# Optimization experiments

Hardware: AMD Instinct MI355X
Metric: run time of the kernel (lower is better)

Reference implementation:

```python
import jax, jax.numpy as jnp
import numpy as np

K = 20          # neighbors
EPS = 1e-5      # BatchNorm eps
SLOPE = 0.2     # LeakyReLU negative slope


def setup_inputs() -> dict:
    key = jax.random.key(0)
    k1, k2 = jax.random.split(key)
    B, C, N, O = 8, 64, 4096, 64
    x = jax.random.normal(k1, (B, C, N), dtype=jnp.float32)
    # 1x1 Conv2d(2C -> O, bias=False) kernel, squeezed to (O, 2C)
    W = jax.random.normal(k2, (O, 2 * C), dtype=jnp.float32) * 0.05
    gamma = jnp.ones((O,), jnp.float32)   # BN weight
    beta = jnp.zeros((O,), jnp.float32)   # BN bias
    return {"x": x, "W": W, "gamma": gamma, "beta": beta}


def _edgeconv(x, W, gamma, beta):
    B, C, N = x.shape
    xt = jnp.transpose(x, (0, 2, 1))                       # (B, N, C)
    # KNN on negative squared distance (matches torch topk of -dist)
    xx = jnp.sum(x * x, axis=1)                            # (B, N)
    inner = jnp.einsum('bnc,bmc->bnm', xt, xt)             # (B, N, N)
    neg_dist = 2.0 * inner - xx[:, :, None] - xx[:, None, :]
    _, idx = jax.lax.top_k(neg_dist, K)                    # (B, N, K) int32
    # gather neighbor features: nbr[b,n,k,c] = xt[b, idx[b,n,k], c]
    nbr = xt[jnp.arange(B)[:, None, None], idx]            # (B, N, K, C)
    center = jnp.broadcast_to(xt[:, :, None, :], (B, N, K, C))
    edge = jnp.concatenate([nbr - center, center], axis=-1)  # (B, N, K, 2C)
    # 1x1 conv == channel matmul
    y = jnp.einsum('bnkc,oc->bnko', edge, W)               # (B, N, K, O)
    # BatchNorm2d (training mode: batch statistics over B,N,K per channel)
    mean = jnp.mean(y, axis=(0, 1, 2))
    var = jnp.var(y, axis=(0, 1, 2))
    yn = (y - mean) * jax.lax.rsqrt(var + EPS) * gamma + beta
    ya = jnp.where(yn >= 0, yn, SLOPE * yn)                # LeakyReLU(0.2)
    out = jnp.max(ya, axis=2)                              # max over k -> (B, N, O)
    return jnp.transpose(out, (0, 2, 1))                   # (B, O, N)


def reference(x, W, gamma, beta):
    return _edgeconv(x, W, gamma, beta)
```

## Files before the change

### kernel.cpp

```cpp
#include <hip/hip_runtime.h>
#include <hip/hip_bf16.h>
#include <math.h>

#define B 8
#define C 64
#define NN 4096
#define O 64
#define KNN 20

typedef float f32x4 __attribute__((ext_vector_type(4)));
typedef short short8_t __attribute__((ext_vector_type(8)));

__device__ inline uint32_t fkey(float f) {
    uint32_t u = __float_as_uint(f);
    return u ^ (((uint32_t)((int32_t)u >> 31)) | 0x80000000u);
}

__device__ inline uint32_t med3u(uint32_t a, uint32_t b, uint32_t c) {
    uint32_t r;
    asm("v_med3_u32 %0, %1, %2, %3" : "=v"(r) : "v"(a), "v"(b), "v"(c));
    return r;
}
__device__ inline uint32_t umax(uint32_t a, uint32_t b) { return a > b ? a : b; }
__device__ inline uint32_t umin(uint32_t a, uint32_t b) { return a < b ? a : b; }

__device__ inline uint32_t minall16(uint32_t v) {
    uint32_t t;
    t = (uint32_t)__builtin_amdgcn_update_dpp(0, (int)v, 0x140, 0xF, 0xF, true);
    v = umin(v, t);
    t = (uint32_t)__builtin_amdgcn_update_dpp(0, (int)v, 0x141, 0xF, 0xF, true);
    v = umin(v, t);
    t = (uint32_t)__builtin_amdgcn_update_dpp(0, (int)v, 0x4E, 0xF, 0xF, true);
    v = umin(v, t);
    t = (uint32_t)__builtin_amdgcn_update_dpp(0, (int)v, 0xB1, 0xF, 0xF, true);
    v = umin(v, t);
    return v;
}


__global__ __launch_bounds__(256) void k1_split(const float* __restrict__ x,
                                                float* __restrict__ xt,
                                                __hip_bfloat16* __restrict__ xh,
                                                float* __restrict__ xx) {
    __shared__ float tile[64][65];
    int b  = blockIdx.x / (NN / 64);
    int n0 = (blockIdx.x % (NN / 64)) * 64;
    int t = threadIdx.x;
    #pragma unroll
    for (int it = 0; it < 16; ++it) {
        int i = it * 256 + t;
        int c = i >> 6, n = i & 63;
        tile[c][n] = x[(size_t)b * C * NN + (size_t)c * NN + n0 + n];
    }
    __syncthreads();
    #pragma unroll
    for (int it = 0; it < 16; ++it) {
        int i = it * 256 + t;
        int n = i >> 6, c = i & 63;
        float v = tile[c][n];
        xt[((size_t)(b * NN + n0 + n)) * C + c] = v;
        int tl   = (n0 + n) >> 4;
        int r    = n & 15;
        int half = c >> 5, cc = c & 31;
        int grp  = cc >> 3, e = cc & 7;
        size_t ta = (size_t)b * NN * 64 + (size_t)tl * 1024 + half * 512
                  + grp * 128 + r * 8 + e;
        xh[ta] = __float2bfloat16(v);
    }
    if (t < 64) {
        float s = 0.f;
        #pragma unroll
        for (int c = 0; c < 64; ++c) { float v = tile[c][t]; s = fmaf(v, v, s); }
        xx[(size_t)b * NN + t + n0] = s;
    }
}

__global__ __launch_bounds__(256) void k2_knn(const __hip_bfloat16* __restrict__ xh,
                                              const float* __restrict__ xt,
                                              const float* __restrict__ xx,
                                              int* __restrict__ idx) {
    int b     = blockIdx.x & 7;
    int qbase = (blockIdx.x >> 3) << 6;
    int t = threadIdx.x;
    int w = t >> 6, lane = t & 63;
    int laneid = lane & 15, grp = lane >> 4;
    int n0w = qbase + w * 16;

    const __hip_bfloat16* xhtb = xh + (size_t)b * NN * 64;
    const float* xxb = xx + (size_t)b * NN;
    const float* xtb = xt + (size_t)b * NN * 64;

    const __hip_bfloat16* lp = xhtb + lane * 8;

    {
    }
    short8_t Ah0 = *(const short8_t*)(lp + (size_t)(n0w >> 4) * 1024);
    short8_t Ah1 = *(const short8_t*)(lp + (size_t)(n0w >> 4) * 1024 + 512);

    float bq[4];
    #pragma unroll
    for (int j = 0; j < 4; ++j) bq[j] = -2.f - xxb[n0w + grp * 4 + j];

    uint32_t qq[4][12];
    #pragma unroll
    for (int j = 0; j < 4; ++j)
        #pragma unroll
        for (int i = 0; i < 12; ++i) qq[j][i] = 0xFFFFFFFFu;

    short8_t P00, P01, P10, P11, P20, P21, P30, P31;
    float Px0, Px1, Px2, Px3;
    P00 = *(const short8_t*)(lp);        P01 = *(const short8_t*)(lp + 512);
    P10 = *(const short8_t*)(lp + 1024); P11 = *(const short8_t*)(lp + 1536);
    P20 = *(const short8_t*)(lp + 2048); P21 = *(const short8_t*)(lp + 2560);
    P30 = *(const short8_t*)(lp + 3072); P31 = *(const short8_t*)(lp + 3584);
    Px0 = xxb[laneid];      Px1 = xxb[laneid + 16];
    Px2 = xxb[laneid + 32]; Px3 = xxb[laneid + 48];

#define SWEEP_BODY(PB0, PB1, PXX, K, PF, OFF)                                  \
    {                                                                          \
        float xxc = PXX;                                                       \
        f32x4 acc = {0.f, 0.f, 0.f, 0.f};                                      \
        acc = __builtin_amdgcn_mfma_f32_16x16x32_bf16(Ah0, PB0, acc, 0, 0, 0); \
        acc = __builtin_amdgcn_mfma_f32_16x16x32_bf16(Ah1, PB1, acc, 0, 0, 0); \
        PB0 = *(const short8_t*)(PF + OFF);                                    \
        PB1 = *(const short8_t*)(PF + OFF + 512);                              \
        PXX = xxb[ci0 + (4 + K) * 16];                                         \
        uint32_t ci = (uint32_t)(ci0 + K * 16);                                \
        _Pragma("unroll")                                                      \
        for (int j = 0; j < 4; ++j) {                                          \
            uint32_t u = __float_as_uint(fmaf(acc[j], 2.f, bq[j] - xxc));      \
            uint32_t nv = (u & 0xFFFFF000u) | ci;                              \
            _Pragma("unroll")                                                  \
            for (int i = 11; i >= 1; --i)                                      \
                qq[j][i] = med3u(qq[j][i - 1], qq[j][i], nv);                  \
            qq[j][0] = umin(qq[j][0], nv);                                     \
        }                                                                      \
    }

    #pragma unroll 1
    for (int tt = 0; tt < 256; tt += 4) {
        int ci0 = tt * 16 + laneid;
        const __hip_bfloat16* pf0 = lp + (size_t)(tt + 4) * 1024;
        const __hip_bfloat16* pf2 = pf0 + 2048;
        SWEEP_BODY(P00, P01, Px0, 0, pf0, 0)
        SWEEP_BODY(P10, P11, Px1, 1, pf0, 1024)
        SWEEP_BODY(P20, P21, Px2, 2, pf2, 0)
        SWEEP_BODY(P30, P31, Px3, 3, pf2, 1024)
    }
#undef SWEEP_BODY

    __shared__ uint32_t cand[4][16][33];
    __shared__ uint32_t rkk[4][16][33];
    __shared__ float qrow[4][16][68];

    #pragma unroll
    for (int i = 0; i < 16; ++i)
        qrow[w][i][lane] = xtb[(size_t)(n0w + i) * 64 + lane];

    #pragma unroll 1
    for (int r = 0; r < 32; ++r) {
        #pragma unroll
        for (int j = 0; j < 4; ++j) {
            uint32_t bk = minall16(qq[j][0]);
            bool win = (qq[j][0] == bk);
            #pragma unroll
            for (int i = 0; i < 11; ++i) qq[j][i] = win ? qq[j][i + 1] : qq[j][i];
            qq[j][11] = win ? 0xFFFFFFFFu : qq[j][11];
            if (laneid == 0) cand[w][grp * 4 + j][r] = bk & 4095u;
        }
    }
    __syncthreads();

    int rq = lane >> 2, rs = lane & 3;
    float qxx = xxb[n0w + rq];
    const float4* qr = (const float4*)qrow[w][rq];
    uint32_t ky[8], cl[8];
    #pragma unroll
    for (int e = 0; e < 8; ++e) {
        uint32_t col = cand[w][rq][rs + 4 * e];
        const float4* cr = (const float4*)(xtb + (size_t)col * 64);
        float a = 0.f;
        #pragma unroll
        for (int i = 0; i < 16; ++i) {
            float4 qv = qr[i], cv = cr[i];
            a = fmaf(qv.x, cv.x, a); a = fmaf(qv.y, cv.y, a);
            a = fmaf(qv.z, cv.z, a); a = fmaf(qv.w, cv.w, a);
        }
        float d = 2.f * a - qxx - xxb[col];
        ky[e] = fkey(d);
        cl[e] = col;
        rkk[w][rq][rs + 4 * e] = ky[e];
    }
    __syncthreads();

    int rank[8];
    #pragma unroll
    for (int e = 0; e < 8; ++e) rank[e] = 0;
    #pragma unroll
    for (int jj = 0; jj < 32; ++jj) {
        uint32_t kj = rkk[w][rq][jj], cj = cand[w][rq][jj];
        #pragma unroll
        for (int e = 0; e < 8; ++e)
            rank[e] += (kj > ky[e] || (kj == ky[e] && cj < cl[e])) ? 1 : 0;
    }
    size_t ob = ((size_t)(b * NN) + n0w + rq) * KNN;
    #pragma unroll
    for (int e = 0; e < 8; ++e)
        if (rank[e] < KNN) idx[ob + rank[e]] = (int)cl[e];
}

__global__ __launch_bounds__(256) void k3a_gemm(const float* __restrict__ xt,
                                                const float* __restrict__ W,
                                                float* __restrict__ Z,
                                                float* __restrict__ Z2) {
    __shared__ float W0t[64][65];
    __shared__ float W21t[64][65];
    __shared__ float xs[16][64];
    int t = threadIdx.x;
    #pragma unroll
    for (int it = 0; it < 16; ++it) {
        int i = it * 256 + t;
        int o = i >> 6, c = i & 63;
        float w0 = W[o * 128 + c];
        float w1 = W[o * 128 + 64 + c];
        W0t[c][o]  = w0;
        W21t[c][o] = w1 - w0;
    }
    int b  = blockIdx.x / (NN / 16);
    int nb = (blockIdx.x % (NN / 16)) * 16;
    #pragma unroll
    for (int it = 0; it < 4; ++it) {
        int i = it * 256 + t;
        int r = i >> 6, c = i & 63;
        xs[r][c] = xt[((size_t)(b * NN + nb + r)) * C + c];
    }
    __syncthreads();
    int o = t & 63, rg = t >> 6;
    #pragma unroll
    for (int rr = 0; rr < 4; ++rr) {
        int r = rg * 4 + rr;
        float z = 0.f, z2 = 0.f;
        #pragma unroll
        for (int c = 0; c < 64; ++c) {
            float xv = xs[r][c];
            z  = fmaf(xv, W0t[c][o],  z);
            z2 = fmaf(xv, W21t[c][o], z2);
        }
        size_t off = ((size_t)(b * NN + nb + r)) * 64 + o;
        Z[off]  = z;
        Z2[off] = z2;
    }
}

__global__ __launch_bounds__(256) void k3b_gather(const float* __restrict__ Z,
                                                  const float* __restrict__ Z2,
                                                  const int* __restrict__ idx,
                                                  float* __restrict__ maxY,
                                                  float* __restrict__ minY,
                                                  float* __restrict__ partials) {
    int t = threadIdx.x;
    int p = t >> 6, o = t & 63;
    int b = blockIdx.x & 7;
    int n = (blockIdx.x >> 3) * 4 + p;
    size_t base = (size_t)(b * NN + n);
    float z2 = Z2[base * 64 + o];
    __shared__ int sidx[4][KNN];
    if (o < KNN) sidx[p][o] = idx[base * KNN + o];
    __syncthreads();
    const float* Zb = Z + (size_t)b * NN * 64;
    float s1 = 0.f, s2 = 0.f, mx = -INFINITY, mn = INFINITY;
    #pragma unroll
    for (int k = 0; k < KNN; ++k) {
        float y = Zb[(size_t)sidx[p][k] * 64 + o] + z2;
        s1 += y;
        s2 = fmaf(y, y, s2);
        mx = fmaxf(mx, y);
        mn = fminf(mn, y);
    }
    maxY[base * 64 + o] = mx;
    minY[base * 64 + o] = mn;
    __shared__ float red[2][4][64];
    red[0][p][o] = s1;
    red[1][p][o] = s2;
    __syncthreads();
    if (t < 64) {
        float a = red[0][0][t] + red[0][1][t] + red[0][2][t] + red[0][3][t];
        float c = red[1][0][t] + red[1][1][t] + red[1][2][t] + red[1][3][t];
        partials[(size_t)blockIdx.x * 128 + t]      = a;
        partials[(size_t)blockIdx.x * 128 + 64 + t] = c;
    }
}

__global__ __launch_bounds__(256) void k4a_reduce(const float* __restrict__ partials,
                                                  float* __restrict__ partials2) {
    int g = blockIdx.x;
    int t = threadIdx.x;
    int col = t & 127, half = t >> 7;
    float s = 0.f;
    for (int r = half; r < 128; r += 2)
        s += partials[((size_t)g * 128 + r) * 128 + col];
    __shared__ float red[2][128];
    red[half][col] = s;
    __syncthreads();
    if (t < 128) partials2[(size_t)g * 128 + t] = red[0][t] + red[1][t];
}

__global__ __launch_bounds__(128) void k4b_stats(const float* __restrict__ partials2,
                                                 const float* __restrict__ gamma,
                                                 const float* __restrict__ beta,
                                                 float* __restrict__ ss) {
    int t = threadIdx.x;
    double s = 0.0;
    for (int i = 0; i < 64; ++i)
        s += (double)partials2[(size_t)i * 128 + t];
    __shared__ double red[128];
    red[t] = s;
    __syncthreads();
    if (t < 64) {
        double a = red[t], c = red[64 + t];
        double M = (double)B * NN * KNN;
        double mean = a / M;
        double var  = c / M - mean * mean;
        float sc = gamma[t] * rsqrtf((float)var + 1e-5f);
        float sh = beta[t] - (float)mean * sc;
        ss[t]      = sc;
        ss[64 + t] = sh;
    }
}

__global__ __launch_bounds__(256) void k5_out(const float* __restrict__ maxY,
                                              const float* __restrict__ minY,
                                              const float* __restrict__ ss,
                                              float* __restrict__ out) {
    __shared__ float tile[64][65];
    __shared__ float sc[64], sh[64];
    int t = threadIdx.x;
    if (t < 64) { sc[t] = ss[t]; sh[t] = ss[64 + t]; }
    int b  = blockIdx.x / (NN / 64);
    int n0 = (blockIdx.x % (NN / 64)) * 64;
    __syncthreads();
    #pragma unroll
    for (int it = 0; it < 16; ++it) {
        int i = it * 256 + t;
        int nl = i >> 6, o = i & 63;
        size_t off = ((size_t)(b * NN + n0 + nl)) * 64 + o;
        float s = sc[o];
        float v = (s >= 0.f) ? maxY[off] : minY[off];
        v = fmaf(v, s, sh[o]);
        v = (v >= 0.f) ? v : 0.2f * v;
        tile[nl][o] = v;
    }
    __syncthreads();
    #pragma unroll
    for (int it = 0; it < 16; ++it) {
        int i = it * 256 + t;
        int o = i >> 6, nl = i & 63;
        out[((size_t)(b * O + o)) * NN + n0 + nl] = tile[nl][o];
    }
}

extern "C" void kernel_launch(void* const* d_in, const int* in_sizes, int n_in,
                              void* d_out, int out_size, void* d_ws, size_t ws_size,
                              hipStream_t stream) {
    const float* x     = (const float*)d_in[0];
    const float* W     = (const float*)d_in[1];
    const float* gamma = (const float*)d_in[2];
    const float* beta  = (const float*)d_in[3];
    float* out = (float*)d_out;

    float* ws = (float*)d_ws;
    float* xx = ws;
    float* xt = xx + (size_t)B * NN;
    __hip_bfloat16* xh = (__hip_bfloat16*)(xt + (size_t)B * NN * C);
    int*   idx = (int*)(xh + (size_t)B * NN * C);
    float* Z   = (float*)(idx + (size_t)B * NN * KNN);
    float* Z2  = Z + (size_t)B * NN * O;
    float* maxY = Z2 + (size_t)B * NN * O;
    float* minY = maxY + (size_t)B * NN * O;
    float* partials  = minY + (size_t)B * NN * O;
    float* partials2 = partials + (size_t)(B * NN / 4) * 128;
    float* ss = partials2 + 64 * 128;

    k1_split<<<B * (NN / 64), 256, 0, stream>>>(x, xt, xh, xx);
    k2_knn<<<B * (NN / 64), 256, 0, stream>>>(xh, xt, xx, idx);
    k3a_gemm<<<B * (NN / 16), 256, 0, stream>>>(xt, W, Z, Z2);
    k3b_gather<<<B * (NN / 4), 256, 0, stream>>>(Z, Z2, idx, maxY, minY, partials);
    k4a_reduce<<<64, 256, 0, stream>>>(partials, partials2);
    k4b_stats<<<1, 128, 0, stream>>>(partials2, gamma, beta, ss);
    k5_out<<<B * (NN / 64), 256, 0, stream>>>(maxY, minY, ss, out);
}
```

Baseline: 235.3 us.

## Split KNN candidate sweep across wave pairs and merge partial candidate lists

```diff
diff --git a/kernel.cpp b/kernel.cpp
--- a/kernel.cpp
+++ b/kernel.cpp
@@ -80,20 +80,21 @@
                                               const float* __restrict__ xx,
                                               int* __restrict__ idx) {
     int b     = blockIdx.x & 7;
-    int qbase = (blockIdx.x >> 3) << 6;
+    int n0blk = (blockIdx.x >> 3) << 5;
     int t = threadIdx.x;
     int w = t >> 6, lane = t & 63;
     int laneid = lane & 15, grp = lane >> 4;
-    int n0w = qbase + w * 16;
+    int pairq = w >> 1, strip = w & 1;
+    int n0w = n0blk + pairq * 16;
+    int s0  = strip * 2048;
 
     const __hip_bfloat16* xhtb = xh + (size_t)b * NN * 64;
     const float* xxb = xx + (size_t)b * NN;
     const float* xtb = xt + (size_t)b * NN * 64;
 
-    const __hip_bfloat16* lp = xhtb + lane * 8;
-
-    {
-    }
+    const __hip_bfloat16* lp  = xhtb + lane * 8;
+    const __hip_bfloat16* lps = lp + (size_t)strip * 128 * 1024;
+
     short8_t Ah0 = *(const short8_t*)(lp + (size_t)(n0w >> 4) * 1024);
     short8_t Ah1 = *(const short8_t*)(lp + (size_t)(n0w >> 4) * 1024 + 512);
 
@@ -109,12 +110,12 @@
 
     short8_t P00, P01, P10, P11, P20, P21, P30, P31;
     float Px0, Px1, Px2, Px3;
-    P00 = *(const short8_t*)(lp);        P01 = *(const short8_t*)(lp + 512);
-    P10 = *(const short8_t*)(lp + 1024); P11 = *(const short8_t*)(lp + 1536);
-    P20 = *(const short8_t*)(lp + 2048); P21 = *(const short8_t*)(lp + 2560);
-    P30 = *(const short8_t*)(lp + 3072); P31 = *(const short8_t*)(lp + 3584);
-    Px0 = xxb[laneid];      Px1 = xxb[laneid + 16];
-    Px2 = xxb[laneid + 32]; Px3 = xxb[laneid + 48];
+    P00 = *(const short8_t*)(lps);        P01 = *(const short8_t*)(lps + 512);
+    P10 = *(const short8_t*)(lps + 1024); P11 = *(const short8_t*)(lps + 1536);
+    P20 = *(const short8_t*)(lps + 2048); P21 = *(const short8_t*)(lps + 2560);
+    P30 = *(const short8_t*)(lps + 3072); P31 = *(const short8_t*)(lps + 3584);
+    Px0 = xxb[s0 + laneid];      Px1 = xxb[s0 + laneid + 16];
+    Px2 = xxb[s0 + laneid + 32]; Px3 = xxb[s0 + laneid + 48];
 
 #define SWEEP_BODY(PB0, PB1, PXX, K, PF, OFF)                                  \
     {                                                                          \
@@ -138,9 +139,9 @@
     }
 
     #pragma unroll 1
-    for (int tt = 0; tt < 256; tt += 4) {
-        int ci0 = tt * 16 + laneid;
-        const __hip_bfloat16* pf0 = lp + (size_t)(tt + 4) * 1024;
+    for (int tt = 0; tt < 128; tt += 4) {
+        int ci0 = s0 + tt * 16 + laneid;
+        const __hip_bfloat16* pf0 = lps + (size_t)(tt + 4) * 1024;
         const __hip_bfloat16* pf2 = pf0 + 2048;
         SWEEP_BODY(P00, P01, Px0, 0, pf0, 0)
         SWEEP_BODY(P10, P11, Px1, 1, pf0, 1024)
@@ -151,11 +152,13 @@
 
     __shared__ uint32_t cand[4][16][33];
     __shared__ uint32_t rkk[4][16][33];
-    __shared__ float qrow[4][16][68];
-
-    #pragma unroll
-    for (int i = 0; i < 16; ++i)
-        qrow[w][i][lane] = xtb[(size_t)(n0w + i) * 64 + lane];
+    __shared__ float qrow[2][16][68];
+
+    if (strip == 0) {
+        #pragma unroll
+        for (int i = 0; i < 16; ++i)
+            qrow[pairq][i][lane] = xtb[(size_t)(n0w + i) * 64 + lane];
+    }
 
     #pragma unroll 1
     for (int r = 0; r < 32; ++r) {
@@ -173,7 +176,7 @@
 
     int rq = lane >> 2, rs = lane & 3;
     float qxx = xxb[n0w + rq];
-    const float4* qr = (const float4*)qrow[w][rq];
+    const float4* qr = (const float4*)qrow[pairq][rq];
     uint32_t ky[8], cl[8];
     #pragma unroll
     for (int e = 0; e < 8; ++e) {
@@ -193,12 +196,14 @@
     }
     __syncthreads();
 
+    int wp0 = w & ~1;
     int rank[8];
     #pragma unroll
     for (int e = 0; e < 8; ++e) rank[e] = 0;
     #pragma unroll
-    for (int jj = 0; jj < 32; ++jj) {
-        uint32_t kj = rkk[w][rq][jj], cj = cand[w][rq][jj];
+    for (int jj = 0; jj < 64; ++jj) {
+        int wp = wp0 + (jj >> 5), slot = jj & 31;
+        uint32_t kj = rkk[wp][rq][slot], cj = cand[wp][rq][slot];
         #pragma unroll
         for (int e = 0; e < 8; ++e)
             rank[e] += (kj > ky[e] || (kj == ky[e] && cj < cl[e])) ? 1 : 0;
@@ -382,7 +387,7 @@
     float* ss = partials2 + 64 * 128;
 
     k1_split<<<B * (NN / 64), 256, 0, stream>>>(x, xt, xh, xx);
-    k2_knn<<<B * (NN / 64), 256, 0, stream>>>(xh, xt, xx, idx);
+    k2_knn<<<B * (NN / 32), 256, 0, stream>>>(xh, xt, xx, idx);
     k3a_gemm<<<B * (NN / 16), 256, 0, stream>>>(xt, W, Z, Z2);
     k3b_gather<<<B * (NN / 4), 256, 0, stream>>>(Z, Z2, idx, maxY, minY, partials);
     k4a_reduce<<<64, 256, 0, stream>>>(partials, partials2);
```

Result: slower. 250.3 us (+6.3%).
